# Optimization experiments

Measured on AMD Instinct MI355X. Metric: run time of the kernel, lower is better.

## Reference

```python
import jax, jax.numpy as jnp
from jax import lax
import numpy as np

B, C, H, W = 2, 128, 64, 64
E = 3            # num_experts
DSTATE = 64      # d_state
DCONV = 4        # d_conv
DIN = 2 * C      # d_inner (expand=2)
DTR = 8          # dt_rank = ceil(C/16)
CONVDIM = 64     # router hidden channels


def mamba_block(xseq, in_w, conv_w, conv_b, xproj_w, dt_w, dt_b, A_log, D, out_w):
    # xseq: (B, L, C)
    Bn, L, _ = xseq.shape
    xr = xseq @ in_w.T                      # (B, L, 2*DIN)
    x, res = jnp.split(xr, 2, axis=-1)
    # depthwise causal conv over sequence dim
    xt = x.transpose(0, 2, 1)               # (B, DIN, L)
    xt = lax.conv_general_dilated(xt, conv_w, window_strides=(1,),
                                  padding=[(DCONV - 1, 0)],
                                  feature_group_count=DIN,
                                  dimension_numbers=('NCW', 'OIW', 'NCW'))
    xt = xt + conv_b[None, :, None]
    x = jax.nn.silu(xt.transpose(0, 2, 1))  # (B, L, DIN)
    # input-dependent SSM params
    dbl = x @ xproj_w.T                     # (B, L, DTR + 2*DSTATE)
    dt, Bm, Cm = dbl[..., :DTR], dbl[..., DTR:DTR + DSTATE], dbl[..., DTR + DSTATE:]
    delta = jax.nn.softplus(dt @ dt_w.T + dt_b)  # (B, L, DIN)
    A = -jnp.exp(A_log)                     # (DIN, DSTATE)

    def step(h, inp):
        d_t, B_t, C_t, u_t = inp            # (B,DIN),(B,DSTATE),(B,DSTATE),(B,DIN)
        dA = jnp.exp(d_t[..., None] * A)    # (B, DIN, DSTATE)
        h = dA * h + (d_t * u_t)[..., None] * B_t[:, None, :]
        y = jnp.einsum('bdn,bn->bd', h, C_t)
        return h, y

    h0 = jnp.zeros((Bn, DIN, DSTATE), x.dtype)
    xs = (delta.transpose(1, 0, 2), Bm.transpose(1, 0, 2),
          Cm.transpose(1, 0, 2), x.transpose(1, 0, 2))
    _, ys = lax.scan(step, h0, xs)          # ys: (L, B, DIN)
    y = ys.transpose(1, 0, 2) + x * D       # skip connection
    y = y * jax.nn.silu(res)                # gate
    return y @ out_w.T                      # (B, L, C)


def setup_inputs() -> dict:
    key = jax.random.key(0)
    ks = jax.random.split(key, 10)
    s = 0.02
    n = lambda k, sh: jax.random.normal(k, sh, jnp.float32) * s
    A_log = jnp.log(jnp.broadcast_to(jnp.arange(1, DSTATE + 1, dtype=jnp.float32),
                                     (E, DIN, DSTATE))) + 0.0
    return {
        'x': jax.random.normal(ks[0], (B, C, H, W), jnp.float32),
        'expert_in_w': n(ks[1], (E, 2 * DIN, C)),
        'expert_conv_w': n(ks[2], (E, DIN, 1, DCONV)),
        'expert_conv_b': jnp.zeros((E, DIN), jnp.float32),
        'expert_xproj_w': n(ks[3], (E, DTR + 2 * DSTATE, DIN)),
        'expert_dt_w': n(ks[4], (E, DIN, DTR)),
        'expert_dt_b': jnp.zeros((E, DIN), jnp.float32),
        'expert_A_log': A_log,
        'expert_D': jnp.ones((E, DIN), jnp.float32),
        'expert_out_w': n(ks[5], (E, C, DIN)),
        'router_conv_w': n(ks[6], (CONVDIM, C, 3, 3)),
        'router_conv_b': jnp.zeros((CONVDIM,), jnp.float32),
        'router_lin_w': n(ks[7], (E, CONVDIM)),
        'router_lin_b': jnp.zeros((E,), jnp.float32),
        'fusion_w': n(ks[8], (C, C)),
        'fusion_b': jnp.zeros((C,), jnp.float32),
    }


def reference(x, expert_in_w, expert_conv_w, expert_conv_b, expert_xproj_w,
              expert_dt_w, expert_dt_b, expert_A_log, expert_D, expert_out_w,
              router_conv_w, router_conv_b, router_lin_w, router_lin_b,
              fusion_w, fusion_b):
    Bn, Cn, Hn, Wn = x.shape
    xseq = x.reshape(Bn, Cn, Hn * Wn).transpose(0, 2, 1)  # (B, L, C)
    # router: conv3x3 -> relu -> global avg pool -> linear -> softmax
    r = lax.conv_general_dilated(x, router_conv_w, (1, 1), 'SAME',
                                 dimension_numbers=('NCHW', 'OIHW', 'NCHW'))
    r = jax.nn.relu(r + router_conv_b[None, :, None, None])
    pooled = r.mean(axis=(2, 3))                          # (B, CONVDIM)
    weights = jax.nn.softmax(pooled @ router_lin_w.T + router_lin_b, axis=1)  # (B, E)
    # run all experts via vmap over the expert axis
    outs = jax.vmap(mamba_block, in_axes=(None, 0, 0, 0, 0, 0, 0, 0, 0, 0))(
        xseq, expert_in_w, expert_conv_w, expert_conv_b, expert_xproj_w,
        expert_dt_w, expert_dt_b, expert_A_log, expert_D, expert_out_w)  # (E,B,L,C)
    outs = outs.transpose(0, 1, 3, 2).reshape(outs.shape[0], Bn, Cn, Hn, Wn)
    ws = jnp.einsum('ebchw,be->bchw', outs, weights)
    out = jnp.einsum('bchw,oc->bohw', ws, fusion_w) + fusion_b[None, :, None, None]
    return out
```

## Files before the change

### kernel.cpp

```cpp
#include <hip/hip_runtime.h>
#include <math.h>
#include <stdint.h>

#define LSEQ 4096
#define NCHUNK 8
#define TC 512

#define AS1 __attribute__((address_space(1)))
#define AS3 __attribute__((address_space(3)))
__device__ __forceinline__ void gload_lds16(const void* g, void* l) {
  __builtin_amdgcn_global_load_lds((const AS1 unsigned int*)g,
                                   (AS3 unsigned int*)l, 16, 0, 0);
}

#define EXP2R(X) __builtin_amdgcn_exp2f(X)

__global__ __launch_bounds__(256) void k_router_conv(
    const float* __restrict__ x, const float* __restrict__ rcw,
    const float* __restrict__ rcb, float* __restrict__ rpool) {
  int bid = blockIdx.x;
  int ocq = bid & 3;
  int h = (bid >> 2) & 63;
  int b = bid >> 8;
  __shared__ float xs[16][3][66];
  __shared__ float wl[16][145];
  int tid = threadIdx.x;
  int ocl = tid & 15;
  int oc = ocq * 16 + ocl;
  int w0 = (tid >> 4) * 4;
  if (tid < 96) {
    int ic = tid / 6, rr = tid % 6;
    int row = rr >> 1, edge = (rr & 1) ? 65 : 0;
    xs[ic][row][edge] = 0.f;
  }
  float acc[4] = {};
  for (int cc = 0; cc < 8; ++cc) {
    __syncthreads();
#pragma unroll
    for (int i = 0; i < 12; ++i) {
      int f = tid + i * 256;
      int ic = f / 192, rem = f % 192;
      int row = rem / 64, w = rem & 63;
      int hh = h - 1 + row;
      float v = 0.f;
      if (hh >= 0 && hh < 64)
        v = x[((size_t)(b * 128 + cc * 16 + ic) * 64 + hh) * 64 + w];
      xs[ic][row][w + 1] = v;
    }
    for (int f = tid; f < 2304; f += 256) {
      int o = f / 144, r = f % 144;
      wl[o][r] = rcw[(size_t)(ocq * 16 + o) * 1152 + cc * 144 + r];
    }
    __syncthreads();
    for (int ic = 0; ic < 16; ++ic) {
#pragma unroll
      for (int kh = 0; kh < 3; ++kh) {
        float xv[6];
#pragma unroll
        for (int j = 0; j < 6; ++j) xv[j] = xs[ic][kh][w0 + j];
        float w_0 = wl[ocl][ic * 9 + kh * 3 + 0];
        float w_1 = wl[ocl][ic * 9 + kh * 3 + 1];
        float w_2 = wl[ocl][ic * 9 + kh * 3 + 2];
#pragma unroll
        for (int i = 0; i < 4; ++i)
          acc[i] += w_0 * xv[i] + w_1 * xv[i + 1] + w_2 * xv[i + 2];
      }
    }
  }
  float cbv = rcb[oc];
  float t = 0.f;
#pragma unroll
  for (int i = 0; i < 4; ++i) t += fmaxf(acc[i] + cbv, 0.f);
  t += __shfl_xor(t, 16);
  t += __shfl_xor(t, 32);
  if ((tid & 63) < 16) atomicAdd(rpool + b * 64 + oc, t);
}

__global__ __launch_bounds__(64) void k_router_softmax(
    const float* __restrict__ rpool, const float* __restrict__ rlw,
    const float* __restrict__ rlb, float* __restrict__ rw) {
  int t = threadIdx.x;
  __shared__ float logits[2][3];
  for (int b = 0; b < 2; ++b) {
    float p = rpool[b * 64 + t] * (1.0f / 4096.0f);
    for (int e = 0; e < 3; ++e) {
      float v = p * rlw[e * 64 + t];
      for (int off = 32; off; off >>= 1) v += __shfl_xor(v, off);
      if (t == 0) logits[b][e] = v + rlb[e];
    }
  }
  __syncthreads();
  if (t == 0) {
    for (int b = 0; b < 2; ++b) {
      float m = fmaxf(fmaxf(logits[b][0], logits[b][1]), logits[b][2]);
      float e0 = expf(logits[b][0] - m), e1 = expf(logits[b][1] - m),
            e2 = expf(logits[b][2] - m);
      float s = e0 + e1 + e2;
      rw[b * 3 + 0] = e0 / s;
      rw[b * 3 + 1] = e1 / s;
      rw[b * 3 + 2] = e2 / s;
    }
  }
}

__global__ __launch_bounds__(256) void k_wfuse(
    const float* __restrict__ fw, const float* __restrict__ outw,
    float* __restrict__ wf) {
  int e = blockIdx.x >> 7;
  int co = blockIdx.x & 127;
  int k = threadIdx.x;
  float acc = 0.f;
  const float* fwr = fw + (size_t)co * 128;
  const float* ob = outw + (size_t)e * 128 * 256 + k;
#pragma unroll 8
  for (int m = 0; m < 128; ++m) acc = fmaf(fwr[m], ob[(size_t)m * 256], acc);
  wf[((size_t)e * 128 + co) * 256 + k] = acc;
}

__global__ __launch_bounds__(256) void k_gemm_in(
    const float* __restrict__ x, const float* __restrict__ inw,
    float* __restrict__ xr) {
  int eb = blockIdx.y;
  int e = eb >> 1, b = eb & 1;
  int lt = blockIdx.x >> 3;
  int jt = blockIdx.x & 7;
  int l0 = lt * 128, j0 = jt * 64;
  __shared__ float xt[16][128];
  __shared__ float wt[16][64];
  int tid = threadIdx.x;
  int jj = (tid & 15) * 4;
  int lr = (tid >> 4) * 8;
  float acc[8][4] = {};
  const float* xb = x + (size_t)b * 128 * 4096;
  const float* wb = inw + (size_t)e * 512 * 128;
  for (int c0 = 0; c0 < 128; c0 += 16) {
    __syncthreads();
#pragma unroll
    for (int i = 0; i < 2; ++i) {
      int f = tid + i * 256;
      int c = f >> 5;
      int lp = (f & 31) * 4;
      float4 v = *(const float4*)(xb + (size_t)(c0 + c) * 4096 + l0 + lp);
      *(float4*)(&xt[c][lp]) = v;
    }
    {
      int j = tid >> 2;
      int kk = (tid & 3) * 4;
      float4 v = *(const float4*)(wb + (size_t)(j0 + j) * 128 + c0 + kk);
      wt[kk + 0][j] = v.x; wt[kk + 1][j] = v.y;
      wt[kk + 2][j] = v.z; wt[kk + 3][j] = v.w;
    }
    __syncthreads();
#pragma unroll
    for (int k = 0; k < 16; ++k) {
      float4 bv = *(const float4*)(&wt[k][jj]);
      float4 a0 = *(const float4*)(&xt[k][lr]);
      float4 a1 = *(const float4*)(&xt[k][lr + 4]);
      float av[8] = {a0.x, a0.y, a0.z, a0.w, a1.x, a1.y, a1.z, a1.w};
#pragma unroll
      for (int i = 0; i < 8; ++i) {
        acc[i][0] = fmaf(av[i], bv.x, acc[i][0]);
        acc[i][1] = fmaf(av[i], bv.y, acc[i][1]);
        acc[i][2] = fmaf(av[i], bv.z, acc[i][2]);
        acc[i][3] = fmaf(av[i], bv.w, acc[i][3]);
      }
    }
  }
  float* out = xr + (size_t)eb * 4096 * 512;
#pragma unroll
  for (int i = 0; i < 8; ++i) {
    float4 v = {acc[i][0], acc[i][1], acc[i][2], acc[i][3]};
    *(float4*)(out + (size_t)(l0 + lr + i) * 512 + j0 + jj) = v;
  }
}

__global__ __launch_bounds__(256) void k_conv1d(
    const float* __restrict__ xr, const float* __restrict__ cw,
    const float* __restrict__ cb, float* __restrict__ xact) {
  int eb = blockIdx.y;
  int e = eb >> 1;
  int l0 = blockIdx.x * 64;
  int d = threadIdx.x;
  const float* w = cw + (size_t)(e * 256 + d) * 4;
  float w0_ = w[0], w1_ = w[1], w2_ = w[2], w3_ = w[3];
  float bias = cb[e * 256 + d];
  const float* xin = xr + (size_t)eb * 4096 * 512 + d;
  float* xo = xact + (size_t)eb * 4096 * 256 + d;
  float xm3 = (l0 >= 3) ? xin[(size_t)(l0 - 3) * 512] : 0.f;
  float xm2 = (l0 >= 2) ? xin[(size_t)(l0 - 2) * 512] : 0.f;
  float xm1 = (l0 >= 1) ? xin[(size_t)(l0 - 1) * 512] : 0.f;
  for (int i = 0; i < 64; ++i) {
    float xc = xin[(size_t)(l0 + i) * 512];
    float v = bias + w0_ * xm3 + w1_ * xm2 + w2_ * xm1 + w3_ * xc;
    xo[(size_t)(l0 + i) * 256] = v / (1.0f + expf(-v));
    xm3 = xm2; xm2 = xm1; xm1 = xc;
  }
}

__global__ __launch_bounds__(256) void k_gemm_xproj(
    const float* __restrict__ xact, const float* __restrict__ xpw,
    float* __restrict__ dbl) {
  int eb = blockIdx.y;
  int e = eb >> 1;
  int lt = blockIdx.x / 3, jt = blockIdx.x % 3;
  int l0 = lt * 128, j0 = jt * 64;
  __shared__ float at[16][128];
  __shared__ float wt[16][64];
  int tid = threadIdx.x;
  int jj = (tid & 15) * 4;
  int lr = (tid >> 4) * 8;
  float acc[8][4] = {};
  const float* ab = xact + (size_t)eb * 4096 * 256;
  const float* wb = xpw + (size_t)e * 136 * 256;
  for (int k0 = 0; k0 < 256; k0 += 16) {
    __syncthreads();
#pragma unroll
    for (int i = 0; i < 2; ++i) {
      int f = tid + i * 256;
      int l = f >> 2, kq = (f & 3) * 4;
      float4 v = *(const float4*)(ab + (size_t)(l0 + l) * 256 + k0 + kq);
      at[kq + 0][l] = v.x; at[kq + 1][l] = v.y;
      at[kq + 2][l] = v.z; at[kq + 3][l] = v.w;
    }
    {
      int j = tid >> 2, kk = (tid & 3) * 4;
      float4 v = {0, 0, 0, 0};
      if (j0 + j < 136)
        v = *(const float4*)(wb + (size_t)(j0 + j) * 256 + k0 + kk);
      wt[kk + 0][j] = v.x; wt[kk + 1][j] = v.y;
      wt[kk + 2][j] = v.z; wt[kk + 3][j] = v.w;
    }
    __syncthreads();
#pragma unroll
    for (int k = 0; k < 16; ++k) {
      float4 bv = *(const float4*)(&wt[k][jj]);
      float4 a0 = *(const float4*)(&at[k][lr]);
      float4 a1 = *(const float4*)(&at[k][lr + 4]);
      float av[8] = {a0.x, a0.y, a0.z, a0.w, a1.x, a1.y, a1.z, a1.w};
#pragma unroll
      for (int i = 0; i < 8; ++i) {
        acc[i][0] = fmaf(av[i], bv.x, acc[i][0]);
        acc[i][1] = fmaf(av[i], bv.y, acc[i][1]);
        acc[i][2] = fmaf(av[i], bv.z, acc[i][2]);
        acc[i][3] = fmaf(av[i], bv.w, acc[i][3]);
      }
    }
  }
  float* ob = dbl + (size_t)eb * 4096 * 136;
  for (int i = 0; i < 8; ++i)
    for (int q = 0; q < 4; ++q) {
      int j = j0 + jj + q;
      if (j < 136) ob[(size_t)(l0 + lr + i) * 136 + j] = acc[i][q];
    }
}

__global__ __launch_bounds__(256) void k_delta(
    const float* __restrict__ dbl, const float* __restrict__ dtw,
    const float* __restrict__ dtb, const float* __restrict__ xact,
    float* __restrict__ dd) {
  int eb = blockIdx.y;
  int e = eb >> 1;
  int t0 = blockIdx.x * 64;
  int d = threadIdx.x;
  __shared__ float dt8[64][8];
  {
    int f = threadIdx.x;
    for (int i = 0; i < 2; ++i, f += 256) {
      int l = f >> 3, r = f & 7;
      dt8[l][r] = dbl[(size_t)eb * 4096 * 136 + (size_t)(t0 + l) * 136 + r];
    }
  }
  __syncthreads();
  float w[8];
#pragma unroll
  for (int r = 0; r < 8; ++r) w[r] = dtw[(size_t)(e * 256 + d) * 8 + r];
  float bias = dtb[e * 256 + d];
  const float* xa = xact + (size_t)eb * 4096 * 256 + d;
  float4* out = (float4*)dd + (size_t)(eb * 256 + d) * 2048 + (t0 >> 1);
  for (int i = 0; i < 64; i += 2) {
    float v0 = bias, v1 = bias;
#pragma unroll
    for (int r = 0; r < 8; ++r) {
      v0 += dt8[i][r] * w[r];
      v1 += dt8[i + 1][r] * w[r];
    }
    float de0 = fmaxf(v0, 0.f) + log1pf(expf(-fabsf(v0)));
    float de1 = fmaxf(v1, 0.f) + log1pf(expf(-fabsf(v1)));
    float u0 = xa[(size_t)(t0 + i) * 256];
    float u1 = xa[(size_t)(t0 + i + 1) * 256];
    float4 o = {de0, de0 * u0, de1, de1 * u1};
    out[i >> 1] = o;
  }
}

#define S1STEP(DVX, DVY, ROW)                    \
  {                                              \
    float Bn = sB[cur][ROW][lane];               \
    h = fmaf(EXP2R((DVX)*An2), h, (DVY)*Bn);     \
    sdel += (DVX);                               \
  }
#define S1HALF(R0, R1, R2, R3, ROFF)             \
  {                                              \
    S1STEP(R0.x, R0.y, (ROFF) + 0)               \
    S1STEP(R0.z, R0.w, (ROFF) + 1)               \
    S1STEP(R1.x, R1.y, (ROFF) + 2)               \
    S1STEP(R1.z, R1.w, (ROFF) + 3)               \
    S1STEP(R2.x, R2.y, (ROFF) + 4)               \
    S1STEP(R2.z, R2.w, (ROFF) + 5)               \
    S1STEP(R3.x, R3.y, (ROFF) + 6)               \
    S1STEP(R3.z, R3.w, (ROFF) + 7)               \
  }

__global__ __launch_bounds__(256, 6) void k_scan1(
    const float* __restrict__ dbl, const float* __restrict__ dd,
    const float* __restrict__ alog, float* __restrict__ prd,
    float* __restrict__ hend) {
  __shared__ float sB[2][16][64];
  int eb = blockIdx.y;
  int e = eb >> 1;
  int c = blockIdx.x >> 6;
  int dgrp = blockIdx.x & 63;
  int wid = threadIdx.x >> 6, lane = threadIdx.x & 63;
  int d = dgrp * 4 + wid;
  float An2 = -__expf(alog[((size_t)e * 256 + d) * 64 + lane]) * 1.44269504f;
  const float2* ddp = (const float2*)dd + ((size_t)eb * 256 + d) * 4096;
  {
    uint64_t a = (uint64_t)ddp;
    uint32_t lo = __builtin_amdgcn_readfirstlane((int)(uint32_t)a);
    uint32_t hi = __builtin_amdgcn_readfirstlane((int)(uint32_t)(a >> 32));
    ddp = (const float2*)(((uint64_t)hi << 32) | (uint64_t)lo);
  }
  const float4* dq = (const float4*)ddp;
  const float* dblb = dbl + (size_t)eb * 4096 * 136;
  int t0 = c * TC;
  int qb = t0 >> 1;
  int srow = 4 * wid + (lane >> 4);
  int scol = (lane & 15) * 4;
  float h = 0.f, sdel = 0.f;
  float4 ra0 = dq[qb + 0], ra1 = dq[qb + 1], ra2 = dq[qb + 2],
         ra3 = dq[qb + 3];
  float4 rb0, rb1, rb2, rb3;
  gload_lds16(dblb + (size_t)(t0 + srow) * 136 + 8 + scol, &sB[0][4 * wid][0]);
  __syncthreads();
  for (int sb = 0; sb < 32; ++sb) {
    int cur = sb & 1;
    if (sb + 1 < 32)
      gload_lds16(dblb + (size_t)(t0 + (sb + 1) * 16 + srow) * 136 + 8 + scol,
                  &sB[cur ^ 1][4 * wid][0]);
    int qA = qb + sb * 8;
    rb0 = dq[qA + 4]; rb1 = dq[qA + 5]; rb2 = dq[qA + 6]; rb3 = dq[qA + 7];
    S1HALF(ra0, ra1, ra2, ra3, 0)
    ra0 = dq[qA + 8]; ra1 = dq[qA + 9]; ra2 = dq[qA + 10]; ra3 = dq[qA + 11];
    S1HALF(rb0, rb1, rb2, rb3, 8)
    __syncthreads();
  }
  size_t o = (((size_t)eb * 256 + d) * NCHUNK + c) * 64 + lane;
  prd[o] = EXP2R(An2 * sdel);
  hend[o] = h;
}

__global__ __launch_bounds__(256) void k_scan2(
    const float* __restrict__ prd, const float* __restrict__ hend,
    float* __restrict__ hinit) {
  int w = blockIdx.x * 4 + (threadIdx.x >> 6);
  int lane = threadIdx.x & 63;
  size_t base = (size_t)w * NCHUNK * 64 + lane;
  float h = 0.f;
  hinit[base] = 0.f;
#pragma unroll
  for (int c = 1; c < NCHUNK; ++c) {
    h = fmaf(prd[base + (c - 1) * 64], h, hend[base + (c - 1) * 64]);
    hinit[base + c * 64] = h;
  }
}

#define S3STEP(DVX, DVY, ROW, JJ)                  \
  {                                                \
    float Bn = sBC[cur][ROW][lane];                \
    float Cn = sBC[cur][ROW][64 + lane];           \
    h = fmaf(EXP2R((DVX)*An2), h, (DVY)*Bn);       \
    P[wid][JJ][lane] = h * Cn;                     \
  }
#define S3HALF(R0, R1, R2, R3, ROFF, TB)           \
  {                                                \
    S3STEP(R0.x, R0.y, (ROFF) + 0, 0)              \
    S3STEP(R0.z, R0.w, (ROFF) + 1, 1)              \
    S3STEP(R1.x, R1.y, (ROFF) + 2, 2)              \
    S3STEP(R1.z, R1.w, (ROFF) + 3, 3)              \
    S3STEP(R2.x, R2.y, (ROFF) + 4, 4)              \
    S3STEP(R2.z, R2.w, (ROFF) + 5, 5)              \
    S3STEP(R3.x, R3.y, (ROFF) + 6, 6)              \
    S3STEP(R3.z, R3.w, (ROFF) + 7, 7)              \
    float acc_ = 0.f;                              \
    _Pragma("unroll")                              \
    for (int k2 = 0; k2 < 8; ++k2)                 \
      acc_ += P[wid][r][q * 8 + k2];               \
    acc_ += __shfl_xor(acc_, 8);                   \
    acc_ += __shfl_xor(acc_, 16);                  \
    acc_ += __shfl_xor(acc_, 32);                  \
    if (lane < 8) yout[(TB) + r] = acc_;           \
  }

__global__ __launch_bounds__(256, 6) void k_scan3(
    const float* __restrict__ dbl, const float* __restrict__ dd,
    const float* __restrict__ alog, const float* __restrict__ hinit,
    float* __restrict__ ytr) {
  __shared__ float sBC[2][16][128];
  __shared__ float P[4][8][65];
  int eb = blockIdx.y;
  int e = eb >> 1;
  int c = blockIdx.x >> 6;
  int dgrp = blockIdx.x & 63;
  int wid = threadIdx.x >> 6, lane = threadIdx.x & 63;
  int d = dgrp * 4 + wid;
  float An2 = -__expf(alog[((size_t)e * 256 + d) * 64 + lane]) * 1.44269504f;
  const float2* ddp = (const float2*)dd + ((size_t)eb * 256 + d) * 4096;
  {
    uint64_t a = (uint64_t)ddp;
    uint32_t lo = __builtin_amdgcn_readfirstlane((int)(uint32_t)a);
    uint32_t hi = __builtin_amdgcn_readfirstlane((int)(uint32_t)(a >> 32));
    ddp = (const float2*)(((uint64_t)hi << 32) | (uint64_t)lo);
  }
  const float4* dq = (const float4*)ddp;
  const float* dblb = dbl + (size_t)eb * 4096 * 136;
  int t0 = c * TC;
  int qb = t0 >> 1;
  int scol = (lane & 31) * 4;
  int srow0 = 4 * wid + (lane >> 5);
  float h = hinit[(((size_t)eb * 256 + d) * NCHUNK + c) * 64 + lane];
  float* yout = ytr + ((size_t)eb * 256 + d) * 4096;
  int r = lane & 7, q = lane >> 3;
  float4 ra0 = dq[qb + 0], ra1 = dq[qb + 1], ra2 = dq[qb + 2],
         ra3 = dq[qb + 3];
  float4 rb0, rb1, rb2, rb3;
  gload_lds16(dblb + (size_t)(t0 + srow0) * 136 + 8 + scol,
              &sBC[0][4 * wid][0]);
  gload_lds16(dblb + (size_t)(t0 + srow0 + 2) * 136 + 8 + scol,
              &sBC[0][4 * wid + 2][0]);
  __syncthreads();
  for (int sb = 0; sb < 32; ++sb) {
    int cur = sb & 1;
    if (sb + 1 < 32) {
      int tN = t0 + (sb + 1) * 16;
      gload_lds16(dblb + (size_t)(tN + srow0) * 136 + 8 + scol,
                  &sBC[cur ^ 1][4 * wid][0]);
      gload_lds16(dblb + (size_t)(tN + srow0 + 2) * 136 + 8 + scol,
                  &sBC[cur ^ 1][4 * wid + 2][0]);
    }
    int qA = qb + sb * 8;
    int tA = t0 + sb * 16;
    rb0 = dq[qA + 4]; rb1 = dq[qA + 5]; rb2 = dq[qA + 6]; rb3 = dq[qA + 7];
    S3HALF(ra0, ra1, ra2, ra3, 0, tA)
    ra0 = dq[qA + 8]; ra1 = dq[qA + 9]; ra2 = dq[qA + 10]; ra3 = dq[qA + 11];
    S3HALF(rb0, rb1, rb2, rb3, 8, tA + 8)
    __syncthreads();
  }
}

__global__ __launch_bounds__(256) void k_yfuse(
    const float* __restrict__ ytr, const float* __restrict__ xact,
    const float* __restrict__ xr, const float* __restrict__ Dw,
    float* __restrict__ yf) {
  int eb = blockIdx.y;
  int e = eb >> 1;
  int dti = blockIdx.x >> 6, tti = blockIdx.x & 63;
  int d0 = dti * 64, t0 = tti * 64;
  __shared__ float sp[64][65];
  __shared__ float sq[64][65];
  int tid = threadIdx.x;
  int j = tid & 63;
  int r0 = tid >> 6;
  float Dj = Dw[e * 256 + d0 + j];
  const float* xab = xact + (size_t)eb * 4096 * 256;
  const float* xrb = xr + (size_t)eb * 4096 * 512;
#pragma unroll
  for (int it = 0; it < 16; ++it) {
    int r = r0 + it * 4;
    float xa = xab[(size_t)(t0 + r) * 256 + d0 + j];
    float rs = xrb[(size_t)(t0 + r) * 512 + 256 + d0 + j];
    float pch = rs / (1.0f + expf(-rs));
    sp[r][j] = pch;
    sq[r][j] = xa * Dj * pch;
  }
  __syncthreads();
#pragma unroll
  for (int it = 0; it < 16; ++it) {
    int ddr = r0 + it * 4;
    size_t idx = ((size_t)eb * 256 + d0 + ddr) * 4096 + t0 + j;
    float y = ytr[idx];
    yf[idx] = y * sp[j][ddr] + sq[j][ddr];
  }
}

__global__ __launch_bounds__(256) void k_gemm_out2(
    const float* __restrict__ yf, const float* __restrict__ wf,
    const float* __restrict__ rw, const float* __restrict__ fb,
    float* __restrict__ out) {
  int b = blockIdx.y;
  int tt = blockIdx.x >> 1;
  int ct = blockIdx.x & 1;
  int t0 = tt * 64, c0 = ct * 64;
  __shared__ float at[16][66];
  __shared__ float wt[16][64];
  int tid = threadIdx.x;
  int co4 = (tid & 15) * 4;
  int t4 = (tid >> 4) * 4;
  float acc[4][4] = {};
  for (int e = 0; e < 3; ++e) {
    float wbe = rw[b * 3 + e];
    const float* ab = yf + (size_t)(e * 2 + b) * 256 * 4096;
    const float* wb = wf + (size_t)e * 128 * 256;
    for (int k0 = 0; k0 < 256; k0 += 16) {
      __syncthreads();
      {
#pragma unroll
        for (int i = 0; i < 4; ++i) {
          int f = tid + i * 256;
          int t = f & 63, k = f >> 6;
          at[k][t] = ab[(size_t)(k0 + k) * 4096 + t0 + t];
        }
        int jc = tid >> 2, kk = (tid & 3) * 4;
        float4 v = *(const float4*)(wb + (size_t)(c0 + jc) * 256 + k0 + kk);
        wt[kk + 0][jc] = v.x * wbe; wt[kk + 1][jc] = v.y * wbe;
        wt[kk + 2][jc] = v.z * wbe; wt[kk + 3][jc] = v.w * wbe;
      }
      __syncthreads();
#pragma unroll
      for (int k = 0; k < 16; ++k) {
        float4 bv = *(const float4*)(&wt[k][co4]);
        float4 av = *(const float4*)(&at[k][t4]);
        float a_[4] = {av.x, av.y, av.z, av.w};
#pragma unroll
        for (int i = 0; i < 4; ++i) {
          acc[i][0] = fmaf(a_[i], bv.x, acc[i][0]);
          acc[i][1] = fmaf(a_[i], bv.y, acc[i][1]);
          acc[i][2] = fmaf(a_[i], bv.z, acc[i][2]);
          acc[i][3] = fmaf(a_[i], bv.w, acc[i][3]);
        }
      }
    }
  }
#pragma unroll
  for (int o = 0; o < 4; ++o) {
    float bias = fb[c0 + co4 + o];
    float4 v = {acc[0][o] + bias, acc[1][o] + bias, acc[2][o] + bias,
                acc[3][o] + bias};
    *(float4*)(out + ((size_t)(b * 128 + c0 + co4 + o)) * 4096 + t0 + t4) = v;
  }
}

extern "C" void kernel_launch(void* const* d_in, const int* in_sizes, int n_in,
                              void* d_out, int out_size, void* d_ws,
                              size_t ws_size, hipStream_t stream) {
  const float* x    = (const float*)d_in[0];
  const float* inw  = (const float*)d_in[1];
  const float* cw   = (const float*)d_in[2];
  const float* cb   = (const float*)d_in[3];
  const float* xpw  = (const float*)d_in[4];
  const float* dtw  = (const float*)d_in[5];
  const float* dtb  = (const float*)d_in[6];
  const float* alog = (const float*)d_in[7];
  const float* Dw   = (const float*)d_in[8];
  const float* outw = (const float*)d_in[9];
  const float* rcw  = (const float*)d_in[10];
  const float* rcb  = (const float*)d_in[11];
  const float* rlw  = (const float*)d_in[12];
  const float* rlb  = (const float*)d_in[13];
  const float* fw   = (const float*)d_in[14];
  const float* fb   = (const float*)d_in[15];

  float* ws = (float*)d_ws;
  float* XR    = ws;
  float* XACT  = ws + 12582912;
  float* DBL   = ws + 18874368;
  float* DD    = ws + 22216704;
  float* YTR   = ws + 34799616;
  float* MIX   = ws + 41091072;
  float* RPOOL = ws + 42139648;
  float* RW    = ws + 42139776;
  float* YF    = DD;
  float* PRD   = YTR;
  float* HEND  = YTR + 786432;
  float* HINIT = MIX;
  float* WF    = MIX + 786432;

  if (ws_size < (size_t)42139784 * sizeof(float)) return;

  hipMemsetAsync(RPOOL, 0, 128 * sizeof(float), stream);
  k_router_conv<<<512, 256, 0, stream>>>(x, rcw, rcb, RPOOL);
  k_router_softmax<<<1, 64, 0, stream>>>(RPOOL, rlw, rlb, RW);
  k_wfuse<<<384, 256, 0, stream>>>(fw, outw, WF);
  k_gemm_in<<<dim3(256, 6), 256, 0, stream>>>(x, inw, XR);
  k_conv1d<<<dim3(64, 6), 256, 0, stream>>>(XR, cw, cb, XACT);
  k_gemm_xproj<<<dim3(96, 6), 256, 0, stream>>>(XACT, xpw, DBL);
  k_delta<<<dim3(64, 6), 256, 0, stream>>>(DBL, dtw, dtb, XACT, DD);
  k_scan1<<<dim3(64 * 7, 6), 256, 0, stream>>>(DBL, DD, alog, PRD, HEND);
  k_scan2<<<384, 256, 0, stream>>>(PRD, HEND, HINIT);
  k_scan3<<<dim3(64 * NCHUNK, 6), 256, 0, stream>>>(DBL, DD, alog, HINIT, YTR);
  k_yfuse<<<dim3(256, 6), 256, 0, stream>>>(YTR, XACT, XR, Dw, YF);
  k_gemm_out2<<<dim3(128, 2), 256, 0, stream>>>(YF, WF, RW, fb, (float*)d_out);
}
```

Measured before the change: 570.5 us.

## Fuse D-skip and SiLU gate epilogue into scan3, split conv1d into more blocks

Removes the separate k_yfuse kernel. scan3 now buffers y values in shared memory and every 64 timesteps applies the D skip connection and the SiLU(res) gate before writing the gated output that the final GEMM reads. This saves one full write and read of the y tensor plus a kernel launch, at the cost of strided xact/xr loads inside the latency-critical scan loop. k_conv1d also uses 16-step chunks with four times as many blocks and an unrolled loop to increase parallelism.

```diff
diff --git a/kernel.cpp b/kernel.cpp
--- a/kernel.cpp
+++ b/kernel.cpp
@@ -14,6 +14,7 @@
 }
 
 #define EXP2R(X) __builtin_amdgcn_exp2f(X)
+#define LOG2E 1.44269504f
 
 __global__ __launch_bounds__(256) void k_router_conv(
     const float* __restrict__ x, const float* __restrict__ rcw,
@@ -179,7 +180,7 @@
     const float* __restrict__ cb, float* __restrict__ xact) {
   int eb = blockIdx.y;
   int e = eb >> 1;
-  int l0 = blockIdx.x * 64;
+  int l0 = blockIdx.x * 16;
   int d = threadIdx.x;
   const float* w = cw + (size_t)(e * 256 + d) * 4;
   float w0_ = w[0], w1_ = w[1], w2_ = w[2], w3_ = w[3];
@@ -189,7 +190,8 @@
   float xm3 = (l0 >= 3) ? xin[(size_t)(l0 - 3) * 512] : 0.f;
   float xm2 = (l0 >= 2) ? xin[(size_t)(l0 - 2) * 512] : 0.f;
   float xm1 = (l0 >= 1) ? xin[(size_t)(l0 - 1) * 512] : 0.f;
-  for (int i = 0; i < 64; ++i) {
+#pragma unroll
+  for (int i = 0; i < 16; ++i) {
     float xc = xin[(size_t)(l0 + i) * 512];
     float v = bias + w0_ * xm3 + w1_ * xm2 + w2_ * xm1 + w3_ * xc;
     xo[(size_t)(l0 + i) * 256] = v / (1.0f + expf(-v));
@@ -322,7 +324,7 @@
   int dgrp = blockIdx.x & 63;
   int wid = threadIdx.x >> 6, lane = threadIdx.x & 63;
   int d = dgrp * 4 + wid;
-  float An2 = -__expf(alog[((size_t)e * 256 + d) * 64 + lane]) * 1.44269504f;
+  float An2 = -__expf(alog[((size_t)e * 256 + d) * 64 + lane]) * LOG2E;
   const float2* ddp = (const float2*)dd + ((size_t)eb * 256 + d) * 4096;
   {
     uint64_t a = (uint64_t)ddp;
@@ -398,22 +400,24 @@
     acc_ += __shfl_xor(acc_, 8);                   \
     acc_ += __shfl_xor(acc_, 16);                  \
     acc_ += __shfl_xor(acc_, 32);                  \
-    if (lane < 8) yout[(TB) + r] = acc_;           \
+    if (lane < 8) yrow[wid][((TB)&63) + r] = acc_; \
   }
 
 __global__ __launch_bounds__(256, 6) void k_scan3(
     const float* __restrict__ dbl, const float* __restrict__ dd,
     const float* __restrict__ alog, const float* __restrict__ hinit,
-    float* __restrict__ ytr) {
+    const float* __restrict__ xact, const float* __restrict__ xr,
+    const float* __restrict__ Dw, float* __restrict__ ytr) {
   __shared__ float sBC[2][16][128];
   __shared__ float P[4][8][65];
+  __shared__ float yrow[4][64];
   int eb = blockIdx.y;
   int e = eb >> 1;
   int c = blockIdx.x >> 6;
   int dgrp = blockIdx.x & 63;
   int wid = threadIdx.x >> 6, lane = threadIdx.x & 63;
   int d = dgrp * 4 + wid;
-  float An2 = -__expf(alog[((size_t)e * 256 + d) * 64 + lane]) * 1.44269504f;
+  float An2 = -__expf(alog[((size_t)e * 256 + d) * 64 + lane]) * LOG2E;
   const float2* ddp = (const float2*)dd + ((size_t)eb * 256 + d) * 4096;
   {
     uint64_t a = (uint64_t)ddp;
@@ -429,6 +433,9 @@
   int srow0 = 4 * wid + (lane >> 5);
   float h = hinit[(((size_t)eb * 256 + d) * NCHUNK + c) * 64 + lane];
   float* yout = ytr + ((size_t)eb * 256 + d) * 4096;
+  const float* xab = xact + (size_t)eb * 4096 * 256 + d;
+  const float* xrb = xr + (size_t)eb * 4096 * 512 + 256 + d;
+  float Dd = Dw[e * 256 + d];
   int r = lane & 7, q = lane >> 3;
   float4 ra0 = dq[qb + 0], ra1 = dq[qb + 1], ra2 = dq[qb + 2],
          ra3 = dq[qb + 3];
@@ -453,42 +460,15 @@
     S3HALF(ra0, ra1, ra2, ra3, 0, tA)
     ra0 = dq[qA + 8]; ra1 = dq[qA + 9]; ra2 = dq[qA + 10]; ra3 = dq[qA + 11];
     S3HALF(rb0, rb1, rb2, rb3, 8, tA + 8)
-    __syncthreads();
-  }
-}
-
-__global__ __launch_bounds__(256) void k_yfuse(
-    const float* __restrict__ ytr, const float* __restrict__ xact,
-    const float* __restrict__ xr, const float* __restrict__ Dw,
-    float* __restrict__ yf) {
-  int eb = blockIdx.y;
-  int e = eb >> 1;
-  int dti = blockIdx.x >> 6, tti = blockIdx.x & 63;
-  int d0 = dti * 64, t0 = tti * 64;
-  __shared__ float sp[64][65];
-  __shared__ float sq[64][65];
-  int tid = threadIdx.x;
-  int j = tid & 63;
-  int r0 = tid >> 6;
-  float Dj = Dw[e * 256 + d0 + j];
-  const float* xab = xact + (size_t)eb * 4096 * 256;
-  const float* xrb = xr + (size_t)eb * 4096 * 512;
-#pragma unroll
-  for (int it = 0; it < 16; ++it) {
-    int r = r0 + it * 4;
-    float xa = xab[(size_t)(t0 + r) * 256 + d0 + j];
-    float rs = xrb[(size_t)(t0 + r) * 512 + 256 + d0 + j];
-    float pch = rs / (1.0f + expf(-rs));
-    sp[r][j] = pch;
-    sq[r][j] = xa * Dj * pch;
-  }
-  __syncthreads();
-#pragma unroll
-  for (int it = 0; it < 16; ++it) {
-    int ddr = r0 + it * 4;
-    size_t idx = ((size_t)eb * 256 + d0 + ddr) * 4096 + t0 + j;
-    float y = ytr[idx];
-    yf[idx] = y * sp[j][ddr] + sq[j][ddr];
+    if ((sb & 3) == 3) {
+      int t = t0 + (sb - 3) * 16 + lane;
+      float yv = yrow[wid][lane];
+      float xa = xab[(size_t)t * 256];
+      float rs = xrb[(size_t)t * 512];
+      float pch = rs * __builtin_amdgcn_rcpf(1.f + EXP2R(-rs * LOG2E));
+      yout[t] = (yv + xa * Dd) * pch;
+    }
+    __syncthreads();
   }
 }
 
@@ -578,7 +558,6 @@
   float* MIX   = ws + 41091072;
   float* RPOOL = ws + 42139648;
   float* RW    = ws + 42139776;
-  float* YF    = DD;
   float* PRD   = YTR;
   float* HEND  = YTR + 786432;
   float* HINIT = MIX;
@@ -591,12 +570,13 @@
   k_router_softmax<<<1, 64, 0, stream>>>(RPOOL, rlw, rlb, RW);
   k_wfuse<<<384, 256, 0, stream>>>(fw, outw, WF);
   k_gemm_in<<<dim3(256, 6), 256, 0, stream>>>(x, inw, XR);
-  k_conv1d<<<dim3(64, 6), 256, 0, stream>>>(XR, cw, cb, XACT);
+  k_conv1d<<<dim3(256, 6), 256, 0, stream>>>(XR, cw, cb, XACT);
   k_gemm_xproj<<<dim3(96, 6), 256, 0, stream>>>(XACT, xpw, DBL);
   k_delta<<<dim3(64, 6), 256, 0, stream>>>(DBL, dtw, dtb, XACT, DD);
   k_scan1<<<dim3(64 * 7, 6), 256, 0, stream>>>(DBL, DD, alog, PRD, HEND);
   k_scan2<<<384, 256, 0, stream>>>(PRD, HEND, HINIT);
-  k_scan3<<<dim3(64 * NCHUNK, 6), 256, 0, stream>>>(DBL, DD, alog, HINIT, YTR);
-  k_yfuse<<<dim3(256, 6), 256, 0, stream>>>(YTR, XACT, XR, Dw, YF);
-  k_gemm_out2<<<dim3(128, 2), 256, 0, stream>>>(YF, WF, RW, fb, (float*)d_out);
-}
+  k_scan3<<<dim3(64 * NCHUNK, 6), 256, 0, stream>>>(DBL, DD, alog, HINIT,
+                                                    XACT, XR, Dw, YTR);
+  k_gemm_out2<<<dim3(128, 2), 256, 0, stream>>>(YTR, WF, RW, fb,
+                                                (float*)d_out);
+}
```

After: 587.9 us. +3.0%, slower.
